# Kernel tuning notes

Measured on AMD Instinct MI355X. Metric: run time of the kernel, lower is better.

Reference implementation:

```python
import jax, jax.numpy as jnp
import numpy as np

S = 3072        # total tokens (3 images x 1024 patches)
E = 1280        # n_embed
H = 16          # n_heads
HD = E // H     # head_dim = 80
NSEG = 3


def rotate_half(x):
    x1 = x[..., : x.shape[-1] // 2]
    x2 = x[..., x.shape[-1] // 2 :]
    return jnp.concatenate((-x2, x1), axis=-1)


def setup_inputs() -> dict:
    key = jax.random.key(0)
    ks = jax.random.split(key, 6)
    x = jax.random.normal(ks[0], (S, E), dtype=jnp.float32)
    rotary_pos_emb = jax.random.normal(ks[1], (S, HD // 2), dtype=jnp.float32)
    qkv_w = jax.random.normal(ks[2], (3 * E, E), dtype=jnp.float32) * 0.02
    qkv_b = jax.random.normal(ks[3], (3 * E,), dtype=jnp.float32) * 0.02
    proj_w = jax.random.normal(ks[4], (E, E), dtype=jnp.float32) * 0.02
    proj_b = jax.random.normal(ks[5], (E,), dtype=jnp.float32) * 0.02
    cu_seqlens = (jnp.arange(NSEG + 1, dtype=jnp.int32) * (S // NSEG))  # [0,1024,2048,3072]
    return {"x": x, "rotary_pos_emb": rotary_pos_emb, "qkv_w": qkv_w,
            "qkv_b": qkv_b, "proj_w": proj_w, "proj_b": proj_b,
            "cu_seqlens": cu_seqlens}


def reference(x, rotary_pos_emb, qkv_w, qkv_b, proj_w, proj_b, cu_seqlens):
    seq_len = x.shape[0]
    # qkv projection (torch Linear: x @ W.T + b)
    qkv = (x @ qkv_w.T + qkv_b).reshape(seq_len, 3, H, HD)
    q, k, v = qkv[:, 0], qkv[:, 1], qkv[:, 2]          # each [S, H, HD]

    # inline RoPE: cos/sin repeated over the two halves of head_dim
    cos = jnp.cos(rotary_pos_emb)
    sin = jnp.sin(rotary_pos_emb)
    cos = jnp.concatenate([cos, cos], axis=-1)[:, None, :]  # [S, 1, HD]
    sin = jnp.concatenate([sin, sin], axis=-1)[:, None, :]
    q = q * cos + rotate_half(q) * sin
    k = k * cos + rotate_half(k) * sin

    # block-diagonal segment mask from cu_seqlens
    seg = jnp.searchsorted(cu_seqlens, jnp.arange(seq_len), side="right")  # [S]
    mask = seg[:, None] == seg[None, :]                 # [S, S] bool

    scale = jnp.asarray(1.0 / np.sqrt(HD), dtype=q.dtype)
    scores = jnp.einsum("qhd,khd->hqk", q, k) * scale   # [H, S, S]
    scores = jnp.where(mask[None], scores, jnp.finfo(scores.dtype).min)
    attn = jax.nn.softmax(scores, axis=-1)
    out = jnp.einsum("hqk,khd->qhd", attn, v).reshape(seq_len, E)
    return out @ proj_w.T + proj_b
```

## Files before the change

kernel.cpp:

```cpp
#include <hip/hip_runtime.h>
#include <hip/hip_bf16.h>
#include <math.h>

#define SEQ   3072
#define EMB   1280
#define NHEAD 16
#define HDIM  80
#define QKVN  3840
#define NSEGS 3

typedef __attribute__((ext_vector_type(8))) short bf16x8;
typedef __attribute__((ext_vector_type(4))) short bf16x4;
typedef __attribute__((ext_vector_type(4))) float f32x4;

__device__ __forceinline__ short f2bf(float f) {
    __hip_bfloat16 h = __float2bfloat16(f);
    return *reinterpret_cast<short*>(&h);
}
__device__ __forceinline__ float bf2f(short s) {
    unsigned int u = ((unsigned int)(unsigned short)s) << 16;
    union { unsigned int u; float f; } c; c.u = u;
    return c.f;
}

__device__ __forceinline__ void gload_lds16(const void* g, void* l) {
    __builtin_amdgcn_global_load_lds(
        (const __attribute__((address_space(1))) unsigned int*)g,
        (__attribute__((address_space(3))) unsigned int*)l, 16, 0, 0);
}

__global__ __launch_bounds__(256)
void cvt3_kernel(const float* __restrict__ a, short* __restrict__ oa, int na8,
                 const float* __restrict__ b, short* __restrict__ ob, int nb8,
                 const float* __restrict__ c, short* __restrict__ oc, int nc8)
{
    int j = blockIdx.x * 256 + threadIdx.x;
    const float* src; short* dst;
    if (j < na8) { src = a; dst = oa; }
    else if ((j -= na8) < nb8) { src = b; dst = ob; }
    else { j -= nb8; src = c; dst = oc; }
    float4 x = *reinterpret_cast<const float4*>(&src[j*8]);
    float4 y = *reinterpret_cast<const float4*>(&src[j*8+4]);
    bf16x8 o;
    o[0]=f2bf(x.x); o[1]=f2bf(x.y); o[2]=f2bf(x.z); o[3]=f2bf(x.w);
    o[4]=f2bf(y.x); o[5]=f2bf(y.y); o[6]=f2bf(y.z); o[7]=f2bf(y.w);
    *reinterpret_cast<bf16x8*>(&dst[j*8]) = o;
}

__device__ __forceinline__ void store_val(float v, float* p) { *p = v; }
__device__ __forceinline__ void store_val(float v, short* p) { *p = f2bf(v); }

template<typename OT>
__global__ __launch_bounds__(256)
void gemm_bf16_nt(const short* __restrict__ A, int lda,
                  const short* __restrict__ B,
                  const float* __restrict__ bias, OT* __restrict__ C,
                  int M, int N, int K)
{
    __shared__ short As[128][32];
    __shared__ short Bs[128][32];

    const int tid = threadIdx.x;
    const int w   = tid >> 6;
    const int l   = tid & 63;
    const int l15 = l & 15;
    const int l4  = l >> 4;
    const int wr  = w >> 1;
    const int wc  = w & 1;
    const int row0 = blockIdx.y * 128;
    const int col0 = blockIdx.x * 128;

    const int srow = l >> 2;
    const int sk   = (l & 3) * 8;

    f32x4 acc[4][4];
    #pragma unroll
    for (int mi = 0; mi < 4; ++mi)
        #pragma unroll
        for (int ni = 0; ni < 4; ++ni) acc[mi][ni] = (f32x4){0.f,0.f,0.f,0.f};

    for (int k0 = 0; k0 < K; k0 += 32) {
        {
            const int c0 = w, c1 = w + 4;
            gload_lds16(&A[(size_t)(row0 + c0*16 + srow) * lda + k0 + sk], &As[c0*16][0]);
            gload_lds16(&A[(size_t)(row0 + c1*16 + srow) * lda + k0 + sk], &As[c1*16][0]);
            gload_lds16(&B[(size_t)(col0 + c0*16 + srow) * K   + k0 + sk], &Bs[c0*16][0]);
            gload_lds16(&B[(size_t)(col0 + c1*16 + srow) * K   + k0 + sk], &Bs[c1*16][0]);
        }
        __syncthreads();

        bf16x8 af[4], bfr[4];
        #pragma unroll
        for (int mi = 0; mi < 4; ++mi)
            af[mi] = *reinterpret_cast<const bf16x8*>(&As[wr*64 + mi*16 + l15][l4*8]);
        #pragma unroll
        for (int ni = 0; ni < 4; ++ni)
            bfr[ni] = *reinterpret_cast<const bf16x8*>(&Bs[wc*64 + ni*16 + l15][l4*8]);

        #pragma unroll
        for (int mi = 0; mi < 4; ++mi)
            #pragma unroll
            for (int ni = 0; ni < 4; ++ni)
                acc[mi][ni] = __builtin_amdgcn_mfma_f32_16x16x32_bf16(
                    af[mi], bfr[ni], acc[mi][ni], 0, 0, 0);
        __syncthreads();
    }

    #pragma unroll
    for (int ni = 0; ni < 4; ++ni) {
        int col = col0 + wc*64 + ni*16 + l15;
        float bv = bias[col];
        #pragma unroll
        for (int mi = 0; mi < 4; ++mi) {
            #pragma unroll
            for (int r = 0; r < 4; ++r) {
                size_t row = (size_t)(row0 + wr*64 + mi*16 + l4*4 + r);
                store_val(acc[mi][ni][r] + bv, &C[row * (size_t)N + col]);
            }
        }
    }
}

__global__ __launch_bounds__(256)
void rope_bf16_kernel(short* __restrict__ qkv, const float* __restrict__ rpe)
{
    int idx = blockIdx.x * 256 + threadIdx.x;
    int blk = idx % 5;
    int h   = (idx / 5) % NHEAD;
    int s   = (idx / (5*NHEAD)) % SEQ;
    int t   = idx / (5*NHEAD*SEQ);
    int d0  = blk * 8;

    const float* rp = rpe + s*40 + d0;
    short* p = qkv + (size_t)s*QKVN + t*EMB + h*HDIM + d0;
    bf16x8 v0 = *reinterpret_cast<const bf16x8*>(p);
    bf16x8 v1 = *reinterpret_cast<const bf16x8*>(p + 40);
    bf16x8 o0, o1;
    #pragma unroll
    for (int j = 0; j < 8; ++j) {
        float ang = rp[j];
        float sn = sinf(ang), cs = cosf(ang);
        float a = bf2f(v0[j]), b = bf2f(v1[j]);
        o0[j] = f2bf(a*cs - b*sn);
        o1[j] = f2bf(b*cs + a*sn);
    }
    *reinterpret_cast<bf16x8*>(p)      = o0;
    *reinterpret_cast<bf16x8*>(p + 40) = o1;
}

__global__ __launch_bounds__(256)
void attn_mfma(const short* __restrict__ qkv, const int* __restrict__ cu,
               short* __restrict__ aout)
{
    const int h   = blockIdx.z;
    const int seg = blockIdx.y;
    const int qt  = blockIdx.x;
    const int s0 = cu[seg], s1 = cu[seg+1];

    const int tid = threadIdx.x;
    const int w   = tid >> 6;
    const int l   = tid & 63;
    const int l15 = l & 15;
    const int l4  = l >> 4;

    __shared__ short Kl[64][128];
    __shared__ short Vt[HDIM][64];

    const int q0 = s0 + qt*64 + w*16;

    bf16x8 bzero;
    #pragma unroll
    for (int j = 0; j < 8; ++j) bzero[j] = 0;

    bf16x8 qf[3];
    {
        const short* qp = qkv + (size_t)(q0 + l15) * QKVN + h*HDIM;
        qf[0] = *reinterpret_cast<const bf16x8*>(qp + l4*8);
        qf[1] = *reinterpret_cast<const bf16x8*>(qp + 32 + l4*8);
        qf[2] = (l4 < 2) ? *reinterpret_cast<const bf16x8*>(qp + 64 + l4*8) : bzero;
    }

    float m = -3.4e38f, lsum = 0.f;
    f32x4 O[5];
    #pragma unroll
    for (int dt = 0; dt < 5; ++dt) O[dt] = (f32x4){0.f,0.f,0.f,0.f};

    int kkey[3], ku[3];
    const short* kptr[3];
    short* klds[3];
    #pragma unroll
    for (int i = 0; i < 3; ++i) {
        int task = tid + i*256;
        kkey[i] = task / 12;
        ku[i]   = task - kkey[i]*12;
        kptr[i] = qkv + (size_t)(s0 + kkey[i])*QKVN + EMB + h*HDIM + ku[i]*8;
        klds[i] = &Kl[kkey[i]][(ku[i] ^ (kkey[i] & 7))*8];
    }

    const int u1  = ((l >> 2) & 3) | ((l >> 5) << 2);
    const int bs1 = ((l >> 4) & 1) * 4 + (l & 3);
    const int k2  = w*16 + l15;
    const int u2  = ((k2 >> 2) & 3) | ((k2 >> 5) << 2);
    const int bs2 = ((k2 >> 4) & 1) * 4 + (k2 & 3);
    const bool sec = (l < 16);

    const short* vp1 = qkv + (size_t)(s0 + l)  * QKVN + 2*EMB + h*HDIM + w*16;
    const short* vp2 = qkv + (size_t)(s0 + k2) * QKVN + 2*EMB + h*HDIM + 64;

    bf16x8 kreg[3];
    bf16x8 vregA, vregB, vregC, vregD;
    #pragma unroll
    for (int i = 0; i < 3; ++i)
        kreg[i] = (ku[i] < 10) ? *reinterpret_cast<const bf16x8*>(kptr[i]) : bzero;
    vregA = *reinterpret_cast<const bf16x8*>(vp1);
    vregB = *reinterpret_cast<const bf16x8*>(vp1 + 8);
    if (sec) {
        vregC = *reinterpret_cast<const bf16x8*>(vp2);
        vregD = *reinterpret_cast<const bf16x8*>(vp2 + 8);
    }

    const float scale2 = 0.1612982054f;
    const int nk = s1 - s0;
    const size_t step = (size_t)64 * QKVN;
    short* vt_flat = &Vt[0][0];

    for (int kc = 0; kc < nk; kc += 64) {
        __syncthreads();

        #pragma unroll
        for (int i = 0; i < 3; ++i)
            *reinterpret_cast<bf16x8*>(klds[i]) = kreg[i];
        {
            const int rb = w*16*64;
            #pragma unroll
            for (int i = 0; i < 8; ++i) {
                vt_flat[rb + i*64      + ((u1 ^ i)       & 7)*8 + bs1] = vregA[i];
                vt_flat[rb + (i+8)*64  + ((u1 ^ i)       & 7)*8 + bs1] = vregB[i];
            }
            if (sec) {
                #pragma unroll
                for (int i = 0; i < 8; ++i) {
                    vt_flat[(64+i)*64  + ((u2 ^ i)       & 7)*8 + bs2] = vregC[i];
                    vt_flat[(72+i)*64  + ((u2 ^ i)       & 7)*8 + bs2] = vregD[i];
                }
            }
        }

        if (kc + 64 < nk) {
            #pragma unroll
            for (int i = 0; i < 3; ++i) {
                kptr[i] += step;
                if (ku[i] < 10) kreg[i] = *reinterpret_cast<const bf16x8*>(kptr[i]);
            }
            vp1 += step; vp2 += step;
            vregA = *reinterpret_cast<const bf16x8*>(vp1);
            vregB = *reinterpret_cast<const bf16x8*>(vp1 + 8);
            if (sec) {
                vregC = *reinterpret_cast<const bf16x8*>(vp2);
                vregD = *reinterpret_cast<const bf16x8*>(vp2 + 8);
            }
        }
        __syncthreads();

        f32x4 S[4];
        __builtin_amdgcn_s_setprio(1);
        #pragma unroll
        for (int ct = 0; ct < 4; ++ct) {
            f32x4 acc = (f32x4){0.f,0.f,0.f,0.f};
            int key = ct*16 + l15;
            #pragma unroll
            for (int t = 0; t < 3; ++t) {
                int u = (4*t + l4) ^ (key & 7);
                bf16x8 a = *reinterpret_cast<const bf16x8*>(&Kl[key][u*8]);
                acc = __builtin_amdgcn_mfma_f32_16x16x32_bf16(a, qf[t], acc, 0, 0, 0);
            }
            S[ct] = acc;
        }
        __builtin_amdgcn_s_setprio(0);

        float mx = -3.4e38f;
        #pragma unroll
        for (int ct = 0; ct < 4; ++ct)
            #pragma unroll
            for (int r = 0; r < 4; ++r) {
                float v = S[ct][r] * scale2;
                S[ct][r] = v;
                mx = fmaxf(mx, v);
            }
        mx = fmaxf(mx, __shfl_xor(mx, 16));
        mx = fmaxf(mx, __shfl_xor(mx, 32));
        if (!__all(mx - m <= 8.f)) {
            float mn   = fmaxf(m, mx);
            float corr = exp2f(m - mn);
            lsum *= corr;
            #pragma unroll
            for (int dt = 0; dt < 5; ++dt)
                #pragma unroll
                for (int r = 0; r < 4; ++r) O[dt][r] *= corr;
            m = mn;
        }
        float p[4][4];
        float ps = 0.f;
        #pragma unroll
        for (int ct = 0; ct < 4; ++ct)
            #pragma unroll
            for (int r = 0; r < 4; ++r) {
                float e = exp2f(S[ct][r] - m);
                p[ct][r] = e;
                ps += e;
            }
        ps += __shfl_xor(ps, 16);
        ps += __shfl_xor(ps, 32);
        lsum += ps;

        #pragma unroll
        for (int s2 = 0; s2 < 2; ++s2) {
            bf16x8 pb;
            #pragma unroll
            for (int j = 0; j < 8; ++j)
                pb[j] = f2bf(p[2*s2 + (j>>2)][j & 3]);
            __builtin_amdgcn_s_setprio(1);
            #pragma unroll
            for (int dt = 0; dt < 5; ++dt) {
                int d = dt*16 + l15;
                bf16x8 va = *reinterpret_cast<const bf16x8*>(
                    &vt_flat[d*64 + (((4*s2 + l4) ^ (d & 7)) & 7)*8]);
                O[dt] = __builtin_amdgcn_mfma_f32_16x16x32_bf16(va, pb, O[dt], 0, 0, 0);
            }
            __builtin_amdgcn_s_setprio(0);
        }
    }

    float inv = 1.f / lsum;
    short* orow = aout + (size_t)(q0 + l15) * EMB + h*HDIM;
    #pragma unroll
    for (int dt = 0; dt < 5; ++dt) {
        bf16x4 o4;
        #pragma unroll
        for (int r = 0; r < 4; ++r) o4[r] = f2bf(O[dt][r] * inv);
        *reinterpret_cast<bf16x4*>(&orow[dt*16 + 4*l4]) = o4;
    }
}

extern "C" void kernel_launch(void* const* d_in, const int* in_sizes, int n_in,
                              void* d_out, int out_size, void* d_ws, size_t ws_size,
                              hipStream_t stream)
{
    const float* x      = (const float*)d_in[0];
    const float* rpe    = (const float*)d_in[1];
    const float* qkv_w  = (const float*)d_in[2];
    const float* qkv_b  = (const float*)d_in[3];
    const float* proj_w = (const float*)d_in[4];
    const float* proj_b = (const float*)d_in[5];
    const int*   cu     = (const int*)d_in[6];
    float* out = (float*)d_out;

    short* ws       = (short*)d_ws;
    short* qkv_bf   = ws;
    short* x_bf     = qkv_bf  + (size_t)SEQ * QKVN;
    short* qkvw_bf  = x_bf    + (size_t)SEQ * EMB;
    short* projw_bf = qkvw_bf + (size_t)QKVN * EMB;
    short* attn_bf  = projw_bf+ (size_t)EMB * EMB;

    dim3 blk(256);

    const int na8 = SEQ*EMB/8, nb8 = QKVN*EMB/8, nc8 = EMB*EMB/8;
    cvt3_kernel<<<dim3((na8+nb8+nc8)/256), blk, 0, stream>>>(
        x, x_bf, na8, qkv_w, qkvw_bf, nb8, proj_w, projw_bf, nc8);

    gemm_bf16_nt<short><<<dim3(QKVN/128, SEQ/128), blk, 0, stream>>>(
        x_bf, EMB, qkvw_bf, qkv_b, qkv_bf, SEQ, QKVN, EMB);

    rope_bf16_kernel<<<dim3(2*SEQ*NHEAD*5/256), blk, 0, stream>>>(qkv_bf, rpe);

    attn_mfma<<<dim3((SEQ/NSEGS)/64, NSEGS, NHEAD), blk, 0, stream>>>(
        qkv_bf, cu, attn_bf);

    gemm_bf16_nt<float><<<dim3(EMB/128, SEQ/128), blk, 0, stream>>>(
        attn_bf, EMB, projw_bf, proj_b, out, SEQ, EMB, EMB);
}
```

Measured before the change: 154.4 us.

## Remap attention blocks to XCDs, fold softmax scale into exp, narrow proj GEMM tile

The attention grid becomes a flat 1D launch whose block index is decoded so that every (head, segment) pair is pinned to one XCD. All 16 query tiles of that pair then share K/V through the same L2. The softmax scale is now applied once to the row max and fused into the exp2 argument with an fma, which removes a per-element multiply pass. The output projection moves to a new 128x64-tile GEMM variant that launches twice as many blocks (480 instead of 240) to fill more CUs, at the cost of less reuse per block.

```diff
diff --git a/kernel.cpp b/kernel.cpp
--- a/kernel.cpp
+++ b/kernel.cpp
@@ -121,6 +121,76 @@
     }
 }
 
+template<typename OT>
+__global__ __launch_bounds__(256)
+void gemm_bf16_nt64(const short* __restrict__ A, int lda,
+                    const short* __restrict__ B,
+                    const float* __restrict__ bias, OT* __restrict__ C,
+                    int M, int N, int K)
+{
+    __shared__ short As[128][32];
+    __shared__ short Bs[64][32];
+
+    const int tid = threadIdx.x;
+    const int w   = tid >> 6;
+    const int l   = tid & 63;
+    const int l15 = l & 15;
+    const int l4  = l >> 4;
+    const int wr  = w >> 1;
+    const int wc  = w & 1;
+    const int row0 = blockIdx.y * 128;
+    const int col0 = blockIdx.x * 64;
+
+    const int srow = l >> 2;
+    const int sk   = (l & 3) * 8;
+
+    f32x4 acc[4][2];
+    #pragma unroll
+    for (int mi = 0; mi < 4; ++mi)
+        #pragma unroll
+        for (int ni = 0; ni < 2; ++ni) acc[mi][ni] = (f32x4){0.f,0.f,0.f,0.f};
+
+    for (int k0 = 0; k0 < K; k0 += 32) {
+        {
+            const int c0 = w, c1 = w + 4;
+            gload_lds16(&A[(size_t)(row0 + c0*16 + srow) * lda + k0 + sk], &As[c0*16][0]);
+            gload_lds16(&A[(size_t)(row0 + c1*16 + srow) * lda + k0 + sk], &As[c1*16][0]);
+            gload_lds16(&B[(size_t)(col0 + w*16  + srow) * K   + k0 + sk], &Bs[w*16][0]);
+        }
+        __syncthreads();
+
+        bf16x8 af[4], bfr[2];
+        #pragma unroll
+        for (int mi = 0; mi < 4; ++mi)
+            af[mi] = *reinterpret_cast<const bf16x8*>(&As[wr*64 + mi*16 + l15][l4*8]);
+        #pragma unroll
+        for (int ni = 0; ni < 2; ++ni)
+            bfr[ni] = *reinterpret_cast<const bf16x8*>(&Bs[wc*32 + ni*16 + l15][l4*8]);
+
+        #pragma unroll
+        for (int mi = 0; mi < 4; ++mi)
+            #pragma unroll
+            for (int ni = 0; ni < 2; ++ni)
+                acc[mi][ni] = __builtin_amdgcn_mfma_f32_16x16x32_bf16(
+                    af[mi], bfr[ni], acc[mi][ni], 0, 0, 0);
+        __syncthreads();
+    }
+
+    #pragma unroll
+    for (int ni = 0; ni < 2; ++ni) {
+        int col = col0 + wc*32 + ni*16 + l15;
+        float bv = bias[col];
+        #pragma unroll
+        for (int mi = 0; mi < 4; ++mi) {
+            #pragma unroll
+            for (int r = 0; r < 4; ++r) {
+                size_t row = (size_t)(row0 + wr*64 + mi*16 + l4*4 + r);
+                store_val(acc[mi][ni][r] + bv, &C[row * (size_t)N + col]);
+            }
+        }
+    }
+}
+
 __global__ __launch_bounds__(256)
 void rope_bf16_kernel(short* __restrict__ qkv, const float* __restrict__ rpe)
 {
@@ -152,9 +222,14 @@
 void attn_mfma(const short* __restrict__ qkv, const int* __restrict__ cu,
                short* __restrict__ aout)
 {
-    const int h   = blockIdx.z;
-    const int seg = blockIdx.y;
-    const int qt  = blockIdx.x;
+    const int flat = blockIdx.x;
+    const int xcd  = flat & 7;
+    const int rem  = flat >> 3;
+    const int qt   = rem & 15;
+    const int shhi = rem >> 4;
+    const int sh   = xcd + 8*shhi;
+    const int h    = sh / 3;
+    const int seg  = sh - 3*h;
     const int s0 = cu[seg], s1 = cu[seg+1];
 
     const int tid = threadIdx.x;
@@ -278,15 +353,12 @@
         }
         __builtin_amdgcn_s_setprio(0);
 
-        float mx = -3.4e38f;
+        float mxr = -3.4e38f;
         #pragma unroll
         for (int ct = 0; ct < 4; ++ct)
             #pragma unroll
-            for (int r = 0; r < 4; ++r) {
-                float v = S[ct][r] * scale2;
-                S[ct][r] = v;
-                mx = fmaxf(mx, v);
-            }
+            for (int r = 0; r < 4; ++r) mxr = fmaxf(mxr, S[ct][r]);
+        float mx = mxr * scale2;
         mx = fmaxf(mx, __shfl_xor(mx, 16));
         mx = fmaxf(mx, __shfl_xor(mx, 32));
         if (!__all(mx - m <= 8.f)) {
@@ -305,7 +377,7 @@
         for (int ct = 0; ct < 4; ++ct)
             #pragma unroll
             for (int r = 0; r < 4; ++r) {
-                float e = exp2f(S[ct][r] - m);
+                float e = exp2f(fmaf(S[ct][r], scale2, -m));
                 p[ct][r] = e;
                 ps += e;
             }
@@ -373,9 +445,8 @@
 
     rope_bf16_kernel<<<dim3(2*SEQ*NHEAD*5/256), blk, 0, stream>>>(qkv_bf, rpe);
 
-    attn_mfma<<<dim3((SEQ/NSEGS)/64, NSEGS, NHEAD), blk, 0, stream>>>(
-        qkv_bf, cu, attn_bf);
-
-    gemm_bf16_nt<float><<<dim3(EMB/128, SEQ/128), blk, 0, stream>>>(
+    attn_mfma<<<dim3(16*NSEGS*NHEAD), blk, 0, stream>>>(qkv_bf, cu, attn_bf);
+
+    gemm_bf16_nt64<float><<<dim3(EMB/64, SEQ/128), blk, 0, stream>>>(
         attn_bf, EMB, projw_bf, proj_b, out, SEQ, EMB, EMB);
 }
```

Measured after the change: 144.7 us. 1.07x faster.
